# Kernel optimization log

Measured on AMD Instinct MI355X. Metric: run time of the kernel, lower is better.

Reference implementation:

```python
import jax, jax.numpy as jnp
import numpy as np

T = 5          # temporal_window_size
B = 512        # batch (graphs per timestep)
NA = 16        # num_agents (nodes per graph)
S = 64         # num_belief_states
A = 16         # action_dim
HID = 64       # hidden_dim per head
H = 4          # num_attn_heads
FD = HID * H   # 256, feature_dim
LAT = 128      # latent_dim
N = B * NA     # total nodes per timestep
FIN = S + A    # node feature dim
NEG_SLOPE = 0.2


def _edge_index():
    i, j = np.meshgrid(np.arange(NA), np.arange(NA), indexing='ij')
    m = i != j
    src_l, dst_l = i[m], j[m]                      # 240 intra-clique edges
    off = (np.arange(B) * NA)[:, None]
    src = (src_l[None] + off).ravel()
    dst = (dst_l[None] + off).ravel()
    loops = np.arange(N)                           # PyG GATConv add_self_loops=True
    src = np.concatenate([src, loops])
    dst = np.concatenate([dst, loops])
    return jnp.asarray(np.stack([src, dst]), dtype=jnp.int64)


def setup_inputs() -> dict:
    key = jax.random.key(0)
    ks = jax.random.split(key, 24)
    xav = lambda k, shp: jax.random.normal(k, shp, jnp.float32) * np.float32(np.sqrt(2.0 / (shp[0] + shp[-1])))
    return {
        'signals': jax.random.normal(ks[0], (T, B, S), jnp.float32),
        'neighbor_actions': jax.random.normal(ks[1], (T, B, NA * A), jnp.float32),
        'lin_w0': xav(ks[2], (FD, FIN)),
        'att_src0': xav(ks[3], (H, HID)),
        'att_dst0': xav(ks[4], (H, HID)),
        'bias0': jnp.zeros((FD,), jnp.float32),
        'lin_w1': xav(ks[5], (FD, FD)),
        'att_src1': xav(ks[6], (H, HID)),
        'att_dst1': xav(ks[7], (H, HID)),
        'bias1': jnp.zeros((FD,), jnp.float32),
        'in_proj_w': xav(ks[8], (3 * FD, FD)),
        'in_proj_b': jnp.zeros((3 * FD,), jnp.float32),
        'out_proj_w': xav(ks[9], (FD, FD)),
        'out_proj_b': jnp.zeros((FD,), jnp.float32),
        'w_mean': xav(ks[10], (LAT, FD)),
        'b_mean': jnp.zeros((LAT,), jnp.float32),
        'w_logvar': xav(ks[11], (LAT, FD)),
        'b_logvar': jnp.zeros((LAT,), jnp.float32),
        'w_belief': xav(ks[12], (S, FD)),
        'b_belief': jnp.zeros((S,), jnp.float32),
        'edge_index': _edge_index(),
    }


def _segment_softmax(e, seg, num_segments):
    # e: [E, T, H]; softmax over edges sharing the same target node.
    m = jax.ops.segment_max(e, seg, num_segments=num_segments)
    e = jnp.exp(e - m[seg])
    s = jax.ops.segment_sum(e, seg, num_segments=num_segments)
    return e / s[seg]


def _gat(x, src, dst, w, a_src, a_dst, b):
    # x: [N, T, Fin] -> [N, T, H*HID]   (PyG GATConv, concat heads)
    xl = jnp.einsum('ntf,of->nto', x, w).reshape(N, T, H, HID)
    e_src = jnp.einsum('nthc,hc->nth', xl, a_src)[src]   # [E, T, H]
    e_dst = jnp.einsum('nthc,hc->nth', xl, a_dst)[dst]
    e = jax.nn.leaky_relu(e_src + e_dst, NEG_SLOPE)
    alpha = _segment_softmax(e, dst, N)                  # per-target softmax
    out = jax.ops.segment_sum(alpha[..., None] * xl[src], dst, num_segments=N)
    return out.reshape(N, T, FD) + b


def reference(signals, neighbor_actions, lin_w0, att_src0, att_dst0, bias0,
              lin_w1, att_src1, att_dst1, bias1, in_proj_w, in_proj_b,
              out_proj_w, out_proj_b, w_mean, b_mean, w_logvar, b_logvar,
              w_belief, b_belief, edge_index):
    # --- _construct_graph (vectorized over time window + batch) ---
    acts = neighbor_actions.reshape(T, B, NA, A)
    beliefs = jnp.zeros((T, B, NA, S), signals.dtype).at[:, :, 0, :].set(signals)
    nodes = jnp.concatenate([beliefs, acts], -1).reshape(T, N, FIN)
    nodes = jnp.transpose(nodes, (1, 0, 2))              # [N, T, FIN]
    src, dst = edge_index[0], edge_index[1]
    x = jax.nn.relu(_gat(nodes, src, dst, lin_w0, att_src0, att_dst0, bias0))
    x = jax.nn.relu(_gat(x, src, dst, lin_w1, att_src1, att_dst1, bias1))
    # --- ego-node sequence: nodes 0, NA, 2*NA, ... ---
    seq = x[::NA]                                        # [B, T, FD]
    # --- temporal MultiheadAttention (batch_first, eval) ---
    qkv = seq @ in_proj_w.T + in_proj_b
    q, k, v = jnp.split(qkv, 3, axis=-1)
    dh = FD // H
    q = q.reshape(B, T, H, dh); k = k.reshape(B, T, H, dh); v = v.reshape(B, T, H, dh)
    scores = jnp.einsum('bqhd,bkhd->bhqk', q, k) / jnp.sqrt(jnp.asarray(dh, seq.dtype))
    # torch float attn_mask is ADDITIVE: mask[i,j]=1 if j<=i else 0
    mask = (jnp.arange(T)[:, None] >= jnp.arange(T)[None, :]).astype(seq.dtype)
    attn = jax.nn.softmax(scores + mask[None, None], axis=-1)
    ctx = jnp.einsum('bhqk,bkhd->bqhd', attn, v).reshape(B, T, FD)
    ctx = ctx @ out_proj_w.T + out_proj_b
    feat = ctx[:, -1]                                    # [B, FD]
    # --- heads ---
    mean = feat @ w_mean.T + b_mean
    logvar = feat @ w_logvar.T + b_logvar
    belief = jax.nn.softmax(feat @ w_belief.T + b_belief, axis=-1)
    return (mean, logvar, belief)
```

## Files before the change

kernel.cpp:

```cpp
#include <hip/hip_runtime.h>
#include <hip/hip_bf16.h>


__device__ __forceinline__ float wave_sum64(float v) {
    #pragma unroll
    for (int off = 32; off > 0; off >>= 1) v += __shfl_xor(v, off, 64);
    return v;
}
__device__ __forceinline__ float wave_max64(float v) {
    #pragma unroll
    for (int off = 32; off > 0; off >>= 1) v = fmaxf(v, __shfl_xor(v, off, 64));
    return v;
}

#define FMA4(acc, wv, zv) \
    acc = fmaf((wv).x, (zv).x, acc); acc = fmaf((wv).y, (zv).y, acc); \
    acc = fmaf((wv).z, (zv).z, acc); acc = fmaf((wv).w, (zv).w, acc);

__global__ __launch_bounds__(256) void k_pre(
    const float* __restrict__ w0, const float* __restrict__ w1,
    const float* __restrict__ wip, const float* __restrict__ wop,
    const float* __restrict__ wm, const float* __restrict__ wlv,
    const float* __restrict__ wb,
    const float* __restrict__ as0, const float* __restrict__ ad0,
    const float* __restrict__ as1, const float* __restrict__ ad1,
    float* __restrict__ tws,
    float* __restrict__ u1, float* __restrict__ ud1,
    float* __restrict__ pa0, float* __restrict__ pd0)
{
    const int tid = threadIdx.x;
    if (blockIdx.x < 1680) {
        int i = blockIdx.x * 256 + tid;
        float v; int d;
        if (i < 16384) {
            int k = i & 63, nn = i >> 6;
            v = w0[nn * 80 + k];
            d = (k >> 2) * 1024 + nn * 4 + (k & 3);
        } else if (i < 20480) {
            int j = i - 16384; int k = j & 15, nn = j >> 4;
            v = w0[nn * 80 + 64 + k];
            d = 16384 + (k >> 2) * 1024 + nn * 4 + (k & 3);
        } else if (i < 86016) {
            int j = i - 20480; int k = j & 255, nn = j >> 8;
            v = w1[nn * 256 + k];
            d = 20480 + (k >> 2) * 1024 + nn * 4 + (k & 3);
        } else if (i < 282624) {
            int j = i - 86016; int k = j & 255, nn = j >> 8;
            v = wip[nn * 256 + k];
            d = 86016 + (k >> 2) * 3072 + nn * 4 + (k & 3);
        } else if (i < 348160) {
            int j = i - 282624; int k = j & 255, nn = j >> 8;
            v = wop[nn * 256 + k];
            d = 282624 + (k >> 2) * 1024 + nn * 4 + (k & 3);
        } else {
            int j = i - 348160; int k = j & 255, o = j >> 8;
            if (o < 128)      v = wm[o * 256 + k];
            else if (o < 256) v = wlv[(o - 128) * 256 + k];
            else              v = wb[(o - 256) * 256 + k];
            d = 348160 + (k >> 2) * 1280 + o * 4 + (k & 3);
        }
        tws[d] = v;
        return;
    }
    if (blockIdx.x < 1684) {
        const int h = blockIdx.x - 1680;
        const int k = tid;
        float su = 0.f, sd = 0.f;
        #pragma unroll
        for (int c = 0; c < 64; c++) {
            float wv = w1[(h * 64 + c) * 256 + k];
            su = fmaf(as1[h * 64 + c], wv, su);
            sd = fmaf(ad1[h * 64 + c], wv, sd);
        }
        u1[h * 256 + k] = su;
        ud1[h * 256 + k] = sd;
        return;
    }
    if (tid < 64) {
        int h = tid >> 4, k = tid & 15;
        float su = 0.f, sd = 0.f;
        #pragma unroll
        for (int c = 0; c < 64; c++) {
            float wv = w0[(h * 64 + c) * 80 + 64 + k];
            su = fmaf(as0[h * 64 + c], wv, su);
            sd = fmaf(ad0[h * 64 + c], wv, sd);
        }
        pa0[tid] = su; pd0[tid] = sd;
    }
}

__global__ __launch_bounds__(256, 5) void k_gat(
    const float* __restrict__ sig,
    const float* __restrict__ nact,
    const float* __restrict__ W0sPK,
    const float* __restrict__ W0aPK,
    const float* __restrict__ W1PK,
    const float* __restrict__ u1g, const float* __restrict__ ud1g,
    const float* __restrict__ pa0g, const float* __restrict__ pd0g,
    const float* __restrict__ as0, const float* __restrict__ ad0,
    const float* __restrict__ b0, const float* __restrict__ b1,
    float* __restrict__ seqf)
{
    __shared__ __align__(16) char smem[28288];
    float* actL    = (float*)(smem + 0);
    float* sigL    = (float*)(smem + 1024);
    float* es0w    = (float*)(smem + 1280);
    float* ed0w    = (float*)(smem + 1536);
    float* espL    = (float*)(smem + 1792);
    float* es1L    = (float*)(smem + 2816);
    float* edpL    = (float*)(smem + 3072);
    float* alpha1L = (float*)(smem + 3136);
    float* a0L     = (float*)(smem + 3392);
    float* zL      = (float*)(smem + 7488);
    float* x1L     = (float*)(smem + 11648);

    const int tid = threadIdx.x;
    const int bg = blockIdx.x;
    const int b = bg / 5, g = bg - b * 5;
    const int n = tid, w = tid >> 6, lane = tid & 63;

    const float4* W0sPK4 = (const float4*)W0sPK;

    float4 wv0[8];
    #pragma unroll
    for (int j = 0; j < 8; j++) wv0[j] = W0sPK4[j * 256 + n];
    float4 wa[4];
    {
        const float4* W0aPK4 = (const float4*)W0aPK;
        #pragma unroll
        for (int q = 0; q < 4; q++) wa[q] = W0aPK4[q * 256 + n];
    }
    const float as0n = as0[n];
    const float ad0n = ad0[n];

    if (tid < 16)
        ((float4*)sigL)[tid] = ((const float4*)(sig + (g * 512 + b) * 64))[tid];
    if (tid < 64)
        ((float4*)actL)[tid] = ((const float4*)(nact + (g * 512 + b) * 256))[tid];
    __syncthreads();

    float S = 0.f;
    {
        const float4* sig4 = (const float4*)sigL;
        #pragma unroll
        for (int j = 0; j < 8; j++) {
            float4 sv = sig4[j];
            S = fmaf(wv0[j].x, sv.x, S);
            S = fmaf(wv0[j].y, sv.y, S);
            S = fmaf(wv0[j].z, sv.z, S);
            S = fmaf(wv0[j].w, sv.w, S);
        }
        float4 wv1[8];
        #pragma unroll
        for (int j = 0; j < 8; j++) wv1[j] = W0sPK4[(8 + j) * 256 + n];
        #pragma unroll
        for (int j = 0; j < 8; j++) {
            float4 sv = sig4[8 + j];
            S = fmaf(wv1[j].x, sv.x, S);
            S = fmaf(wv1[j].y, sv.y, S);
            S = fmaf(wv1[j].z, sv.z, S);
            S = fmaf(wv1[j].w, sv.w, S);
        }
    }
    const int m3 = lane >> 2, q3 = lane & 3;
    const float4 pv = ((const float4*)(pa0g + w * 16))[q3];
    const float4 dv = ((const float4*)(pd0g + w * 16))[q3];

    const float sS = wave_sum64(S * as0n);
    const float dS = wave_sum64(S * ad0n);

    {
        const float4 av = ((const float4*)(actL + m3 * 16))[q3];
        float su = av.x * pv.x;
        su = fmaf(av.y, pv.y, su); su = fmaf(av.z, pv.z, su); su = fmaf(av.w, pv.w, su);
        float sd = av.x * dv.x;
        sd = fmaf(av.y, dv.y, sd); sd = fmaf(av.z, dv.z, sd); sd = fmaf(av.w, dv.w, sd);
        su += __shfl_xor(su, 1, 64); su += __shfl_xor(su, 2, 64);
        sd += __shfl_xor(sd, 1, 64); sd += __shfl_xor(sd, 2, 64);
        if (q3 == 0) {
            es0w[w * 16 + m3] = su + ((m3 == 0) ? sS : 0.f);
            ed0w[w * 16 + m3] = sd + ((m3 == 0) ? dS : 0.f);
        }
    }
    {
        const int j = lane >> 2, q = lane & 3;
        const float ej = ed0w[w * 16 + j];
        const float4 ev = ((const float4*)(es0w + w * 16))[q];
        float e0 = ev.x + ej; e0 = (e0 >= 0.f) ? e0 : 0.2f * e0;
        float e1 = ev.y + ej; e1 = (e1 >= 0.f) ? e1 : 0.2f * e1;
        float e2 = ev.z + ej; e2 = (e2 >= 0.f) ? e2 : 0.2f * e2;
        float e3 = ev.w + ej; e3 = (e3 >= 0.f) ? e3 : 0.2f * e3;
        float mx = fmaxf(fmaxf(e0, e1), fmaxf(e2, e3));
        mx = fmaxf(mx, __shfl_xor(mx, 1, 64));
        mx = fmaxf(mx, __shfl_xor(mx, 2, 64));
        e0 = __expf(e0 - mx); e1 = __expf(e1 - mx);
        e2 = __expf(e2 - mx); e3 = __expf(e3 - mx);
        float s = e0 + e1 + e2 + e3;
        s += __shfl_xor(s, 1, 64); s += __shfl_xor(s, 2, 64);
        float inv = 1.f / s;
        ((float4*)(a0L + (w << 8) + j * 16))[q] =
            make_float4(e0 * inv, e1 * inv, e2 * inv, e3 * inv);
    }

    float x1r[16];
    {
        const float4* act4 = (const float4*)actL;
        float xl0r[16];
        #pragma unroll
        for (int s = 0; s < 16; s++) {
            float a = 0.f;
            #pragma unroll
            for (int q = 0; q < 4; q++) {
                float4 av = act4[s * 4 + q];
                FMA4(a, av, wa[q]);
            }
            xl0r[s] = a;
        }
        xl0r[0] += S;
        const float b0v = b0[n];
        const float4* a04 = (const float4*)(a0L + (w << 8));
        #pragma unroll
        for (int j = 0; j < 16; j++) {
            float acc = b0v;
            #pragma unroll
            for (int s4 = 0; s4 < 4; s4++) {
                float4 a4 = a04[j * 4 + s4];
                acc = fmaf(a4.x, xl0r[s4 * 4 + 0], acc);
                acc = fmaf(a4.y, xl0r[s4 * 4 + 1], acc);
                acc = fmaf(a4.z, xl0r[s4 * 4 + 2], acc);
                acc = fmaf(a4.w, xl0r[s4 * 4 + 3], acc);
            }
            x1r[j] = fmaxf(acc, 0.f);
            x1L[j * 260 + n] = x1r[j];
        }
    }
    __syncthreads();

    {
        const int m = tid & 15, h = (tid >> 4) & 3, p = tid >> 6;
        const float4* x4p = (const float4*)(x1L + m * 260 + p * 64);
        const float4* u4p = ((const float4*)u1g) + h * 64 + p * 16;
        float a = 0.f;
        #pragma unroll
        for (int i = 0; i < 16; i++) {
            float4 xv = x4p[i], uv = u4p[i];
            FMA4(a, xv, uv);
        }
        espL[m * 16 + h * 4 + p] = a;
        if (m == 0) {
            const float4* ud4p = ((const float4*)ud1g) + h * 64 + p * 16;
            float ad = 0.f;
            #pragma unroll
            for (int i = 0; i < 16; i++) {
                float4 xv = x4p[i], uv = ud4p[i];
                FMA4(ad, xv, uv);
            }
            edpL[h * 4 + p] = ad;
        }
    }
    __syncthreads();

    if (w == 0) {
        {
            const int m2 = lane >> 2, h = lane & 3;
            const float* e = espL + m2 * 16 + h * 4;
            es1L[m2 * 4 + h] = e[0] + e[1] + e[2] + e[3];
        }
        if (lane < 16) {
            const int h = lane >> 2, q = lane & 3;
            float ej = edpL[h * 4] + edpL[h * 4 + 1] + edpL[h * 4 + 2] + edpL[h * 4 + 3];
            float e[4]; float mx = -1e30f;
            #pragma unroll
            for (int r = 0; r < 4; r++) {
                float x = es1L[(q * 4 + r) * 4 + h] + ej;
                x = (x >= 0.f) ? x : 0.2f * x;
                e[r] = x; mx = fmaxf(mx, x);
            }
            mx = fmaxf(mx, __shfl_xor(mx, 1, 64));
            mx = fmaxf(mx, __shfl_xor(mx, 2, 64));
            float s = 0.f;
            #pragma unroll
            for (int r = 0; r < 4; r++) { e[r] = __expf(e[r] - mx); s += e[r]; }
            s += __shfl_xor(s, 1, 64);
            s += __shfl_xor(s, 2, 64);
            float inv = 1.f / s;
            ((float4*)(alpha1L + h * 16 + q * 4))[0] =
                make_float4(e[0] * inv, e[1] * inv, e[2] * inv, e[3] * inv);
        }
    }
    __syncthreads();

    const float4* W1PK4 = (const float4*)W1PK;
    float4 w1pf[8];
    #pragma unroll
    for (int j = 0; j < 8; j++) w1pf[j] = W1PK4[j * 256 + n];
    const float b1v = b1[n];
    {
        const float4* a14 = (const float4*)alpha1L;
        #pragma unroll
        for (int hh = 0; hh < 4; hh++) {
            float zv = 0.f;
            #pragma unroll
            for (int s4 = 0; s4 < 4; s4++) {
                float4 a4 = a14[hh * 4 + s4];
                zv = fmaf(a4.x, x1r[s4 * 4 + 0], zv);
                zv = fmaf(a4.y, x1r[s4 * 4 + 1], zv);
                zv = fmaf(a4.z, x1r[s4 * 4 + 2], zv);
                zv = fmaf(a4.w, x1r[s4 * 4 + 3], zv);
            }
            zL[hh * 260 + n] = zv;
        }
    }
    __syncthreads();

    {
        const float4* zh = (const float4*)(zL + w * 260);
        float acc = b1v;
        #pragma unroll
        for (int j = 0; j < 8; j++) {
            float4 z4 = zh[j];
            FMA4(acc, w1pf[j], z4);
        }
        #pragma unroll
        for (int io = 1; io < 8; io++) {
            float4 wv[8];
            #pragma unroll
            for (int j = 0; j < 8; j++) wv[j] = W1PK4[(io * 8 + j) * 256 + n];
            #pragma unroll
            for (int j = 0; j < 8; j++) {
                float4 z4 = zh[io * 8 + j];
                FMA4(acc, wv[j], z4);
            }
        }
        seqf[bg * 256 + n] = fmaxf(acc, 0.f);
    }
}

__global__ __launch_bounds__(768) void k_stage2(
    const float* __restrict__ seqf,
    const float* __restrict__ wipPK,
    const float* __restrict__ bip,
    const float* __restrict__ wopPK,
    const float* __restrict__ bop,
    const float* __restrict__ whPK,
    const float* __restrict__ bm, const float* __restrict__ blv,
    const float* __restrict__ bb,
    float* __restrict__ out)
{
    __shared__ float sseq[2][5][256];
    __shared__ float kL[2][5][256], vL[2][5][256], qL[2][256];
    __shared__ float ctxL[2][256], featL[2][256];
    __shared__ float beliefL[2][64];
    const int tid = threadIdx.x;
    const int b0 = blockIdx.x * 2;

    {
        float4* sflat = (float4*)&sseq[0][0][0];
        const float4* src = (const float4*)(seqf + b0 * 1280);
        if (tid < 640) sflat[tid] = src[tid];
    }
    __syncthreads();

    {
        const int kind = tid >> 8, n = tid & 255;
        const float4* wPK = (const float4*)wipPK + tid;
        if (kind == 0) {
            const float4* s0 = (const float4*)&sseq[0][4][0];
            const float4* s1 = (const float4*)&sseq[1][4][0];
            float a0 = 0.f, a1 = 0.f;
            #pragma unroll 8
            for (int k4 = 0; k4 < 64; k4++) {
                float4 wv = wPK[k4 * 768];
                float4 x0 = s0[k4], x1 = s1[k4];
                a0 = fmaf(x0.x, wv.x, a0); a0 = fmaf(x0.y, wv.y, a0);
                a0 = fmaf(x0.z, wv.z, a0); a0 = fmaf(x0.w, wv.w, a0);
                a1 = fmaf(x1.x, wv.x, a1); a1 = fmaf(x1.y, wv.y, a1);
                a1 = fmaf(x1.z, wv.z, a1); a1 = fmaf(x1.w, wv.w, a1);
            }
            float bv = bip[n];
            qL[0][n] = a0 + bv; qL[1][n] = a1 + bv;
        } else {
            float acc[2][5] = {{0.f,0.f,0.f,0.f,0.f},{0.f,0.f,0.f,0.f,0.f}};
            #pragma unroll 4
            for (int k4 = 0; k4 < 64; k4++) {
                float4 wv = wPK[k4 * 768];
                #pragma unroll
                for (int gb = 0; gb < 2; gb++) {
                    #pragma unroll
                    for (int t = 0; t < 5; t++) {
                        float4 sv = ((const float4*)&sseq[gb][t][0])[k4];
                        float a = acc[gb][t];
                        a = fmaf(sv.x, wv.x, a); a = fmaf(sv.y, wv.y, a);
                        a = fmaf(sv.z, wv.z, a); a = fmaf(sv.w, wv.w, a);
                        acc[gb][t] = a;
                    }
                }
            }
            float bv = bip[kind * 256 + n];
            float* dst = (kind == 1) ? &kL[0][0][0] : &vL[0][0][0];
            #pragma unroll
            for (int gb = 0; gb < 2; gb++)
                #pragma unroll
                for (int t = 0; t < 5; t++)
                    dst[gb * 1280 + t * 256 + n] = acc[gb][t] + bv;
        }
    }
    __syncthreads();

    if (tid < 512) {
        const int gb = tid >> 8, col = tid & 255;
        float q4 = qL[gb][col];
        float sc[5];
        #pragma unroll
        for (int t = 0; t < 5; t++)
            sc[t] = wave_sum64(q4 * kL[gb][t][col]) * 0.125f;
        float m = sc[0];
        #pragma unroll
        for (int t = 1; t < 5; t++) m = fmaxf(m, sc[t]);
        float p[5], sum = 0.f;
        #pragma unroll
        for (int t = 0; t < 5; t++) { p[t] = __expf(sc[t] - m); sum += p[t]; }
        float inv = 1.f / sum, cv = 0.f;
        #pragma unroll
        for (int t = 0; t < 5; t++) cv = fmaf(p[t], vL[gb][t][col], cv);
        ctxL[gb][col] = cv * inv;
    }
    __syncthreads();

    if (tid < 512) {
        const int gb = tid >> 8, n = tid & 255;
        const float4* wPK = (const float4*)wopPK + n;
        const float4* c4 = (const float4*)&ctxL[gb][0];
        float acc = 0.f;
        #pragma unroll 8
        for (int k4 = 0; k4 < 64; k4++) {
            float4 wv = wPK[k4 * 256], cv = c4[k4];
            FMA4(acc, wv, cv);
        }
        featL[gb][n] = acc + bop[n];
    }
    __syncthreads();

    if (tid < 640) {
        const int gb = tid / 320, j = tid - gb * 320;
        const float4* wPK = (const float4*)whPK + j;
        const float4* f4 = (const float4*)&featL[gb][0];
        float acc = 0.f;
        #pragma unroll 8
        for (int k4 = 0; k4 < 64; k4++) {
            float4 wv = wPK[k4 * 320], fv = f4[k4];
            FMA4(acc, wv, fv);
        }
        if (j < 128) {
            out[(b0 + gb) * 128 + j] = acc + bm[j];
        } else if (j < 256) {
            out[65536 + (b0 + gb) * 128 + (j - 128)] = acc + blv[j - 128];
        } else {
            beliefL[gb][j - 256] = acc + bb[j - 256];
        }
    }
    __syncthreads();

    if (tid < 128) {
        int gb = tid >> 6, lane = tid & 63;
        float lg = beliefL[gb][lane];
        float m = wave_max64(lg);
        float e = __expf(lg - m);
        float s = wave_sum64(e);
        out[131072 + (b0 + gb) * 64 + lane] = e / s;
    }
}

extern "C" void kernel_launch(void* const* d_in, const int* in_sizes, int n_in,
                              void* d_out, int out_size, void* d_ws, size_t ws_size,
                              hipStream_t stream) {
    const float* sig  = (const float*)d_in[0];
    const float* nact = (const float*)d_in[1];
    const float* w0   = (const float*)d_in[2];
    const float* as0  = (const float*)d_in[3];
    const float* ad0  = (const float*)d_in[4];
    const float* b0   = (const float*)d_in[5];
    const float* w1   = (const float*)d_in[6];
    const float* as1  = (const float*)d_in[7];
    const float* ad1  = (const float*)d_in[8];
    const float* b1   = (const float*)d_in[9];
    const float* wip  = (const float*)d_in[10];
    const float* bip  = (const float*)d_in[11];
    const float* wop  = (const float*)d_in[12];
    const float* bop  = (const float*)d_in[13];
    const float* wm   = (const float*)d_in[14];
    const float* bm   = (const float*)d_in[15];
    const float* wlv  = (const float*)d_in[16];
    const float* blv  = (const float*)d_in[17];
    const float* wb   = (const float*)d_in[18];
    const float* bb   = (const float*)d_in[19];

    float* ws    = (float*)d_ws;
    float* seqf  = ws;
    float* tws   = ws + 655360;
    float* W0sPK = tws;
    float* W0aPK = tws + 16384;
    float* W1PK  = tws + 20480;
    float* wipPK = tws + 86016;
    float* wopPK = tws + 282624;
    float* whPK  = tws + 348160;
    float* u1    = ws + 1085440;
    float* ud1   = ws + 1086464;
    float* pa0   = ws + 1087488;
    float* pd0   = ws + 1087552;

    k_pre   <<<1685, 256, 0, stream>>>(w0, w1, wip, wop, wm, wlv, wb,
                                       as0, ad0, as1, ad1,
                                       tws, u1, ud1, pa0, pd0);
    k_gat   <<<2560, 256, 0, stream>>>(sig, nact, W0sPK, W0aPK, W1PK,
                                       u1, ud1, pa0, pd0, as0, ad0, b0, b1, seqf);
    k_stage2<<<256, 768, 0, stream>>>(seqf, wipPK, bip, wopPK, bop, whPK,
                                      bm, blv, bb, (float*)d_out);
}
```

Measured before the change: 182.4 us.

## Restructure stage2 to 256 threads computing Q/K/V in registers per column

The temporal-attention kernel now runs 256 threads per block instead of 768, and each thread computes the Q, K and V projections for its column in registers. The attention scores are then reduced across waves directly from those registers, so the K/V/Q shared-memory staging and one barrier go away. In exchange each thread does three times the projection work, holds more registers, and the block has less parallelism to hide weight-load latency. The belief head is handled by the first 64 threads in a separate loop.

```diff
diff --git a/kernel.cpp b/kernel.cpp
--- a/kernel.cpp
+++ b/kernel.cpp
@@ -336,7 +336,7 @@
     }
 }
 
-__global__ __launch_bounds__(768) void k_stage2(
+__global__ __launch_bounds__(256) void k_stage2(
     const float* __restrict__ seqf,
     const float* __restrict__ wipPK,
     const float* __restrict__ bip,
@@ -348,115 +348,116 @@
     float* __restrict__ out)
 {
     __shared__ float sseq[2][5][256];
-    __shared__ float kL[2][5][256], vL[2][5][256], qL[2][256];
-    __shared__ float ctxL[2][256], featL[2][256];
+    __shared__ float ctxL[2][256];
+    __shared__ float featL[2][256];
     __shared__ float beliefL[2][64];
     const int tid = threadIdx.x;
     const int b0 = blockIdx.x * 2;
 
     {
-        float4* sflat = (float4*)&sseq[0][0][0];
+        float4* sf = (float4*)&sseq[0][0][0];
         const float4* src = (const float4*)(seqf + b0 * 1280);
-        if (tid < 640) sflat[tid] = src[tid];
-    }
-    __syncthreads();
-
-    {
-        const int kind = tid >> 8, n = tid & 255;
-        const float4* wPK = (const float4*)wipPK + tid;
-        if (kind == 0) {
-            const float4* s0 = (const float4*)&sseq[0][4][0];
-            const float4* s1 = (const float4*)&sseq[1][4][0];
-            float a0 = 0.f, a1 = 0.f;
+        #pragma unroll
+        for (int r = 0; r < 2; r++) sf[r * 256 + tid] = src[r * 256 + tid];
+        if (tid < 128) sf[512 + tid] = src[512 + tid];
+    }
+    __syncthreads();
+
+    float qa[2] = {0.f, 0.f};
+    float ka[2][5] = {{0,0,0,0,0},{0,0,0,0,0}};
+    float va[2][5] = {{0,0,0,0,0},{0,0,0,0,0}};
+    {
+        const float4* x4 = (const float4*)&sseq[0][0][0];
+        const float4* wqp = (const float4*)wipPK + tid;
+        const float4* wkp = wqp + 256;
+        const float4* wvp = wqp + 512;
+        #pragma unroll 2
+        for (int k4 = 0; k4 < 64; k4++) {
+            float4 wqv = wqp[k4 * 768];
+            float4 wkv = wkp[k4 * 768];
+            float4 wvv = wvp[k4 * 768];
+            #pragma unroll
+            for (int gb = 0; gb < 2; gb++) {
+                #pragma unroll
+                for (int t = 0; t < 5; t++) {
+                    float4 xv = x4[gb * 320 + t * 64 + k4];
+                    FMA4(ka[gb][t], wkv, xv);
+                    FMA4(va[gb][t], wvv, xv);
+                    if (t == 4) FMA4(qa[gb], wqv, xv);
+                }
+            }
+        }
+        const float bq = bip[tid], bk = bip[256 + tid], bv = bip[512 + tid];
+        #pragma unroll
+        for (int gb = 0; gb < 2; gb++) {
+            qa[gb] += bq;
+            #pragma unroll
+            for (int t = 0; t < 5; t++) { ka[gb][t] += bk; va[gb][t] += bv; }
+        }
+    }
+
+    #pragma unroll
+    for (int gb = 0; gb < 2; gb++) {
+        float sc[5];
+        #pragma unroll
+        for (int t = 0; t < 5; t++)
+            sc[t] = wave_sum64(qa[gb] * ka[gb][t]) * 0.125f;
+        float m = sc[0];
+        #pragma unroll
+        for (int t = 1; t < 5; t++) m = fmaxf(m, sc[t]);
+        float p[5], sum = 0.f;
+        #pragma unroll
+        for (int t = 0; t < 5; t++) { p[t] = __expf(sc[t] - m); sum += p[t]; }
+        float inv = 1.f / sum, cv = 0.f;
+        #pragma unroll
+        for (int t = 0; t < 5; t++) cv = fmaf(p[t], va[gb][t], cv);
+        ctxL[gb][tid] = cv * inv;
+    }
+    __syncthreads();
+
+    {
+        const float4* wPK = (const float4*)wopPK + tid;
+        #pragma unroll
+        for (int gb = 0; gb < 2; gb++) {
+            const float4* c4 = (const float4*)&ctxL[gb][0];
+            float acc = 0.f;
             #pragma unroll 8
             for (int k4 = 0; k4 < 64; k4++) {
-                float4 wv = wPK[k4 * 768];
-                float4 x0 = s0[k4], x1 = s1[k4];
-                a0 = fmaf(x0.x, wv.x, a0); a0 = fmaf(x0.y, wv.y, a0);
-                a0 = fmaf(x0.z, wv.z, a0); a0 = fmaf(x0.w, wv.w, a0);
-                a1 = fmaf(x1.x, wv.x, a1); a1 = fmaf(x1.y, wv.y, a1);
-                a1 = fmaf(x1.z, wv.z, a1); a1 = fmaf(x1.w, wv.w, a1);
-            }
-            float bv = bip[n];
-            qL[0][n] = a0 + bv; qL[1][n] = a1 + bv;
-        } else {
-            float acc[2][5] = {{0.f,0.f,0.f,0.f,0.f},{0.f,0.f,0.f,0.f,0.f}};
-            #pragma unroll 4
+                float4 wv = wPK[k4 * 256], cv = c4[k4];
+                FMA4(acc, wv, cv);
+            }
+            featL[gb][tid] = acc + bop[tid];
+        }
+    }
+    __syncthreads();
+
+    {
+        const float4* wPK = (const float4*)whPK + tid;
+        #pragma unroll
+        for (int gb = 0; gb < 2; gb++) {
+            const float4* f4 = (const float4*)&featL[gb][0];
+            float acc = 0.f;
+            #pragma unroll 8
             for (int k4 = 0; k4 < 64; k4++) {
-                float4 wv = wPK[k4 * 768];
-                #pragma unroll
-                for (int gb = 0; gb < 2; gb++) {
-                    #pragma unroll
-                    for (int t = 0; t < 5; t++) {
-                        float4 sv = ((const float4*)&sseq[gb][t][0])[k4];
-                        float a = acc[gb][t];
-                        a = fmaf(sv.x, wv.x, a); a = fmaf(sv.y, wv.y, a);
-                        a = fmaf(sv.z, wv.z, a); a = fmaf(sv.w, wv.w, a);
-                        acc[gb][t] = a;
-                    }
+                float4 wv = wPK[k4 * 320], fv = f4[k4];
+                FMA4(acc, wv, fv);
+            }
+            if (tid < 128) out[(b0 + gb) * 128 + tid] = acc + bm[tid];
+            else out[65536 + (b0 + gb) * 128 + (tid - 128)] = acc + blv[tid - 128];
+        }
+        if (tid < 64) {
+            const float4* w2 = (const float4*)whPK + 256 + tid;
+            #pragma unroll
+            for (int gb = 0; gb < 2; gb++) {
+                const float4* f4 = (const float4*)&featL[gb][0];
+                float acc2 = 0.f;
+                #pragma unroll 8
+                for (int k4 = 0; k4 < 64; k4++) {
+                    float4 wv = w2[k4 * 320], fv = f4[k4];
+                    FMA4(acc2, wv, fv);
                 }
-            }
-            float bv = bip[kind * 256 + n];
-            float* dst = (kind == 1) ? &kL[0][0][0] : &vL[0][0][0];
-            #pragma unroll
-            for (int gb = 0; gb < 2; gb++)
-                #pragma unroll
-                for (int t = 0; t < 5; t++)
-                    dst[gb * 1280 + t * 256 + n] = acc[gb][t] + bv;
-        }
-    }
-    __syncthreads();
-
-    if (tid < 512) {
-        const int gb = tid >> 8, col = tid & 255;
-        float q4 = qL[gb][col];
-        float sc[5];
-        #pragma unroll
-        for (int t = 0; t < 5; t++)
-            sc[t] = wave_sum64(q4 * kL[gb][t][col]) * 0.125f;
-        float m = sc[0];
-        #pragma unroll
-        for (int t = 1; t < 5; t++) m = fmaxf(m, sc[t]);
-        float p[5], sum = 0.f;
-        #pragma unroll
-        for (int t = 0; t < 5; t++) { p[t] = __expf(sc[t] - m); sum += p[t]; }
-        float inv = 1.f / sum, cv = 0.f;
-        #pragma unroll
-        for (int t = 0; t < 5; t++) cv = fmaf(p[t], vL[gb][t][col], cv);
-        ctxL[gb][col] = cv * inv;
-    }
-    __syncthreads();
-
-    if (tid < 512) {
-        const int gb = tid >> 8, n = tid & 255;
-        const float4* wPK = (const float4*)wopPK + n;
-        const float4* c4 = (const float4*)&ctxL[gb][0];
-        float acc = 0.f;
-        #pragma unroll 8
-        for (int k4 = 0; k4 < 64; k4++) {
-            float4 wv = wPK[k4 * 256], cv = c4[k4];
-            FMA4(acc, wv, cv);
-        }
-        featL[gb][n] = acc + bop[n];
-    }
-    __syncthreads();
-
-    if (tid < 640) {
-        const int gb = tid / 320, j = tid - gb * 320;
-        const float4* wPK = (const float4*)whPK + j;
-        const float4* f4 = (const float4*)&featL[gb][0];
-        float acc = 0.f;
-        #pragma unroll 8
-        for (int k4 = 0; k4 < 64; k4++) {
-            float4 wv = wPK[k4 * 320], fv = f4[k4];
-            FMA4(acc, wv, fv);
-        }
-        if (j < 128) {
-            out[(b0 + gb) * 128 + j] = acc + bm[j];
-        } else if (j < 256) {
-            out[65536 + (b0 + gb) * 128 + (j - 128)] = acc + blv[j - 128];
-        } else {
-            beliefL[gb][j - 256] = acc + bb[j - 256];
+                beliefL[gb][tid] = acc2 + bb[tid];
+            }
         }
     }
     __syncthreads();
@@ -514,6 +515,6 @@
                                        tws, u1, ud1, pa0, pd0);
     k_gat   <<<2560, 256, 0, stream>>>(sig, nact, W0sPK, W0aPK, W1PK,
                                        u1, ud1, pa0, pd0, as0, ad0, b0, b1, seqf);
-    k_stage2<<<256, 768, 0, stream>>>(seqf, wipPK, bip, wopPK, bop, whPK,
+    k_stage2<<<256, 256, 0, stream>>>(seqf, wipPK, bip, wopPK, bop, whPK,
                                       bm, blv, bb, (float*)d_out);
 }
```

New measurement: 204.2 us. 11.9% more time.

## Process two batch graphs per GAT block to reuse loaded weights

Applied to the files above, without the earlier changes.

Each k_gat block now handles two graphs (two batch indices at the same timestep) instead of one, and the grid is halved. The per-thread weight registers for W0 and the streamed W1 rows are shared across both graphs, so each weight is fetched once and used twice. The final W1 projection accumulates both graphs in one pass. The cost is more shared memory, more registers (launch bounds drop from 5 to 4 blocks per CU), fewer blocks, and a serial loop over the two graphs for the attention stages.

```diff
diff --git a/kernel.cpp b/kernel.cpp
--- a/kernel.cpp
+++ b/kernel.cpp
@@ -89,7 +89,7 @@
     }
 }
 
-__global__ __launch_bounds__(256, 5) void k_gat(
+__global__ __launch_bounds__(256, 4) void k_gat(
     const float* __restrict__ sig,
     const float* __restrict__ nact,
     const float* __restrict__ W0sPK,
@@ -101,25 +101,26 @@
     const float* __restrict__ b0, const float* __restrict__ b1,
     float* __restrict__ seqf)
 {
-    __shared__ __align__(16) char smem[28288];
-    float* actL    = (float*)(smem + 0);
-    float* sigL    = (float*)(smem + 1024);
-    float* es0w    = (float*)(smem + 1280);
-    float* ed0w    = (float*)(smem + 1536);
-    float* espL    = (float*)(smem + 1792);
-    float* es1L    = (float*)(smem + 2816);
-    float* edpL    = (float*)(smem + 3072);
-    float* alpha1L = (float*)(smem + 3136);
-    float* a0L     = (float*)(smem + 3392);
-    float* zL      = (float*)(smem + 7488);
-    float* x1L     = (float*)(smem + 11648);
+    __shared__ __align__(16) char smem[35136];
+    float* actL  = (float*)(smem + 0);
+    float* sigL  = (float*)(smem + 2048);
+    float* es0w  = (float*)(smem + 2560);
+    float* ed0w  = (float*)(smem + 2816);
+    float* espL  = (float*)(smem + 3072);
+    float* edpL  = (float*)(smem + 4096);
+    float* es1w  = (float*)(smem + 4160);
+    float* alphw = (float*)(smem + 5184);
+    float* a0L   = (float*)(smem + 6208);
+    float* x1L   = (float*)(smem + 10304);
+    float* zL    = (float*)(smem + 26944);
 
     const int tid = threadIdx.x;
-    const int bg = blockIdx.x;
-    const int b = bg / 5, g = bg - b * 5;
+    const int blk = blockIdx.x;
+    const int p = blk / 5, g = blk - p * 5;
     const int n = tid, w = tid >> 6, lane = tid & 63;
 
     const float4* W0sPK4 = (const float4*)W0sPK;
+    const float4* W1PK4  = (const float4*)W1PK;
 
     float4 wv0[8];
     #pragma unroll
@@ -133,206 +134,215 @@
     const float as0n = as0[n];
     const float ad0n = ad0[n];
 
-    if (tid < 16)
-        ((float4*)sigL)[tid] = ((const float4*)(sig + (g * 512 + b) * 64))[tid];
-    if (tid < 64)
-        ((float4*)actL)[tid] = ((const float4*)(nact + (g * 512 + b) * 256))[tid];
+    if (tid < 32) {
+        int pr = tid >> 4, q = tid & 15;
+        ((float4*)sigL)[tid] =
+            ((const float4*)sig)[(g * 512 + 2 * p + pr) * 16 + q];
+    }
+    if (tid < 128) {
+        int pr = tid >> 6, q = tid & 63;
+        ((float4*)actL)[tid] =
+            ((const float4*)nact)[(g * 512 + 2 * p + pr) * 64 + q];
+    }
     __syncthreads();
 
-    float S = 0.f;
+    float SA = 0.f, SB = 0.f;
     {
         const float4* sig4 = (const float4*)sigL;
         #pragma unroll
         for (int j = 0; j < 8; j++) {
-            float4 sv = sig4[j];
-            S = fmaf(wv0[j].x, sv.x, S);
-            S = fmaf(wv0[j].y, sv.y, S);
-            S = fmaf(wv0[j].z, sv.z, S);
-            S = fmaf(wv0[j].w, sv.w, S);
+            float4 wv = wv0[j];
+            float4 va = sig4[j], vb = sig4[16 + j];
+            FMA4(SA, wv, va); FMA4(SB, wv, vb);
         }
         float4 wv1[8];
         #pragma unroll
         for (int j = 0; j < 8; j++) wv1[j] = W0sPK4[(8 + j) * 256 + n];
         #pragma unroll
         for (int j = 0; j < 8; j++) {
-            float4 sv = sig4[8 + j];
-            S = fmaf(wv1[j].x, sv.x, S);
-            S = fmaf(wv1[j].y, sv.y, S);
-            S = fmaf(wv1[j].z, sv.z, S);
-            S = fmaf(wv1[j].w, sv.w, S);
+            float4 wv = wv1[j];
+            float4 va = sig4[8 + j], vb = sig4[24 + j];
+            FMA4(SA, wv, va); FMA4(SB, wv, vb);
         }
     }
     const int m3 = lane >> 2, q3 = lane & 3;
     const float4 pv = ((const float4*)(pa0g + w * 16))[q3];
     const float4 dv = ((const float4*)(pd0g + w * 16))[q3];
-
-    const float sS = wave_sum64(S * as0n);
-    const float dS = wave_sum64(S * ad0n);
-
-    {
-        const float4 av = ((const float4*)(actL + m3 * 16))[q3];
-        float su = av.x * pv.x;
-        su = fmaf(av.y, pv.y, su); su = fmaf(av.z, pv.z, su); su = fmaf(av.w, pv.w, su);
-        float sd = av.x * dv.x;
-        sd = fmaf(av.y, dv.y, sd); sd = fmaf(av.z, dv.z, sd); sd = fmaf(av.w, dv.w, sd);
-        su += __shfl_xor(su, 1, 64); su += __shfl_xor(su, 2, 64);
-        sd += __shfl_xor(sd, 1, 64); sd += __shfl_xor(sd, 2, 64);
-        if (q3 == 0) {
-            es0w[w * 16 + m3] = su + ((m3 == 0) ? sS : 0.f);
-            ed0w[w * 16 + m3] = sd + ((m3 == 0) ? dS : 0.f);
-        }
-    }
-    {
-        const int j = lane >> 2, q = lane & 3;
-        const float ej = ed0w[w * 16 + j];
-        const float4 ev = ((const float4*)(es0w + w * 16))[q];
-        float e0 = ev.x + ej; e0 = (e0 >= 0.f) ? e0 : 0.2f * e0;
-        float e1 = ev.y + ej; e1 = (e1 >= 0.f) ? e1 : 0.2f * e1;
-        float e2 = ev.z + ej; e2 = (e2 >= 0.f) ? e2 : 0.2f * e2;
-        float e3 = ev.w + ej; e3 = (e3 >= 0.f) ? e3 : 0.2f * e3;
-        float mx = fmaxf(fmaxf(e0, e1), fmaxf(e2, e3));
-        mx = fmaxf(mx, __shfl_xor(mx, 1, 64));
-        mx = fmaxf(mx, __shfl_xor(mx, 2, 64));
-        e0 = __expf(e0 - mx); e1 = __expf(e1 - mx);
-        e2 = __expf(e2 - mx); e3 = __expf(e3 - mx);
-        float s = e0 + e1 + e2 + e3;
-        s += __shfl_xor(s, 1, 64); s += __shfl_xor(s, 2, 64);
-        float inv = 1.f / s;
-        ((float4*)(a0L + (w << 8) + j * 16))[q] =
-            make_float4(e0 * inv, e1 * inv, e2 * inv, e3 * inv);
-    }
-
-    float x1r[16];
-    {
-        const float4* act4 = (const float4*)actL;
-        float xl0r[16];
-        #pragma unroll
-        for (int s = 0; s < 16; s++) {
-            float a = 0.f;
-            #pragma unroll
-            for (int q = 0; q < 4; q++) {
-                float4 av = act4[s * 4 + q];
-                FMA4(a, av, wa[q]);
-            }
-            xl0r[s] = a;
-        }
-        xl0r[0] += S;
-        const float b0v = b0[n];
-        const float4* a04 = (const float4*)(a0L + (w << 8));
-        #pragma unroll
-        for (int j = 0; j < 16; j++) {
-            float acc = b0v;
-            #pragma unroll
-            for (int s4 = 0; s4 < 4; s4++) {
-                float4 a4 = a04[j * 4 + s4];
-                acc = fmaf(a4.x, xl0r[s4 * 4 + 0], acc);
-                acc = fmaf(a4.y, xl0r[s4 * 4 + 1], acc);
-                acc = fmaf(a4.z, xl0r[s4 * 4 + 2], acc);
-                acc = fmaf(a4.w, xl0r[s4 * 4 + 3], acc);
-            }
-            x1r[j] = fmaxf(acc, 0.f);
-            x1L[j * 260 + n] = x1r[j];
-        }
-    }
-    __syncthreads();
-
-    {
-        const int m = tid & 15, h = (tid >> 4) & 3, p = tid >> 6;
-        const float4* x4p = (const float4*)(x1L + m * 260 + p * 64);
-        const float4* u4p = ((const float4*)u1g) + h * 64 + p * 16;
-        float a = 0.f;
-        #pragma unroll
-        for (int i = 0; i < 16; i++) {
-            float4 xv = x4p[i], uv = u4p[i];
-            FMA4(a, xv, uv);
-        }
-        espL[m * 16 + h * 4 + p] = a;
-        if (m == 0) {
-            const float4* ud4p = ((const float4*)ud1g) + h * 64 + p * 16;
-            float ad = 0.f;
-            #pragma unroll
-            for (int i = 0; i < 16; i++) {
-                float4 xv = x4p[i], uv = ud4p[i];
-                FMA4(ad, xv, uv);
-            }
-            edpL[h * 4 + p] = ad;
-        }
-    }
-    __syncthreads();
-
-    if (w == 0) {
-        {
-            const int m2 = lane >> 2, h = lane & 3;
-            const float* e = espL + m2 * 16 + h * 4;
-            es1L[m2 * 4 + h] = e[0] + e[1] + e[2] + e[3];
-        }
-        if (lane < 16) {
-            const int h = lane >> 2, q = lane & 3;
-            float ej = edpL[h * 4] + edpL[h * 4 + 1] + edpL[h * 4 + 2] + edpL[h * 4 + 3];
-            float e[4]; float mx = -1e30f;
-            #pragma unroll
-            for (int r = 0; r < 4; r++) {
-                float x = es1L[(q * 4 + r) * 4 + h] + ej;
-                x = (x >= 0.f) ? x : 0.2f * x;
-                e[r] = x; mx = fmaxf(mx, x);
-            }
-            mx = fmaxf(mx, __shfl_xor(mx, 1, 64));
-            mx = fmaxf(mx, __shfl_xor(mx, 2, 64));
-            float s = 0.f;
-            #pragma unroll
-            for (int r = 0; r < 4; r++) { e[r] = __expf(e[r] - mx); s += e[r]; }
-            s += __shfl_xor(s, 1, 64);
-            s += __shfl_xor(s, 2, 64);
-            float inv = 1.f / s;
-            ((float4*)(alpha1L + h * 16 + q * 4))[0] =
-                make_float4(e[0] * inv, e[1] * inv, e[2] * inv, e[3] * inv);
-        }
-    }
-    __syncthreads();
-
-    const float4* W1PK4 = (const float4*)W1PK;
+    const float b0v = b0[n];
+    const float b1v = b1[n];
     float4 w1pf[8];
     #pragma unroll
     for (int j = 0; j < 8; j++) w1pf[j] = W1PK4[j * 256 + n];
-    const float b1v = b1[n];
+
+    float Scur = SA;
+    #pragma unroll 1
+    for (int pr = 0; pr < 2; pr++) {
+        const float sS = wave_sum64(Scur * as0n);
+        const float dS = wave_sum64(Scur * ad0n);
+
+        {
+            const float4 av =
+                ((const float4*)(actL + (pr << 8) + m3 * 16))[q3];
+            float su = av.x * pv.x;
+            su = fmaf(av.y, pv.y, su); su = fmaf(av.z, pv.z, su); su = fmaf(av.w, pv.w, su);
+            float sd = av.x * dv.x;
+            sd = fmaf(av.y, dv.y, sd); sd = fmaf(av.z, dv.z, sd); sd = fmaf(av.w, dv.w, sd);
+            su += __shfl_xor(su, 1, 64); su += __shfl_xor(su, 2, 64);
+            sd += __shfl_xor(sd, 1, 64); sd += __shfl_xor(sd, 2, 64);
+            if (q3 == 0) {
+                es0w[w * 16 + m3] = su + ((m3 == 0) ? sS : 0.f);
+                ed0w[w * 16 + m3] = sd + ((m3 == 0) ? dS : 0.f);
+            }
+        }
+        {
+            const int j = lane >> 2, q = lane & 3;
+            const float ej = ed0w[w * 16 + j];
+            const float4 ev = ((const float4*)(es0w + w * 16))[q];
+            float e0 = ev.x + ej; e0 = (e0 >= 0.f) ? e0 : 0.2f * e0;
+            float e1 = ev.y + ej; e1 = (e1 >= 0.f) ? e1 : 0.2f * e1;
+            float e2 = ev.z + ej; e2 = (e2 >= 0.f) ? e2 : 0.2f * e2;
+            float e3 = ev.w + ej; e3 = (e3 >= 0.f) ? e3 : 0.2f * e3;
+            float mx = fmaxf(fmaxf(e0, e1), fmaxf(e2, e3));
+            mx = fmaxf(mx, __shfl_xor(mx, 1, 64));
+            mx = fmaxf(mx, __shfl_xor(mx, 2, 64));
+            e0 = __expf(e0 - mx); e1 = __expf(e1 - mx);
+            e2 = __expf(e2 - mx); e3 = __expf(e3 - mx);
+            float s = e0 + e1 + e2 + e3;
+            s += __shfl_xor(s, 1, 64); s += __shfl_xor(s, 2, 64);
+            float inv = 1.f / s;
+            ((float4*)(a0L + (w << 8) + j * 16))[q] =
+                make_float4(e0 * inv, e1 * inv, e2 * inv, e3 * inv);
+        }
+
+        float x1r[16];
+        {
+            const float4* act4 = (const float4*)(actL + (pr << 8));
+            float xl0r[16];
+            #pragma unroll
+            for (int s = 0; s < 16; s++) {
+                float a = 0.f;
+                #pragma unroll
+                for (int q = 0; q < 4; q++) {
+                    float4 av = act4[s * 4 + q];
+                    FMA4(a, av, wa[q]);
+                }
+                xl0r[s] = a;
+            }
+            xl0r[0] += Scur;
+            const float4* a04 = (const float4*)(a0L + (w << 8));
+            #pragma unroll
+            for (int j = 0; j < 16; j++) {
+                float acc = b0v;
+                #pragma unroll
+                for (int s4 = 0; s4 < 4; s4++) {
+                    float4 a4 = a04[j * 4 + s4];
+                    acc = fmaf(a4.x, xl0r[s4 * 4 + 0], acc);
+                    acc = fmaf(a4.y, xl0r[s4 * 4 + 1], acc);
+                    acc = fmaf(a4.z, xl0r[s4 * 4 + 2], acc);
+                    acc = fmaf(a4.w, xl0r[s4 * 4 + 3], acc);
+                }
+                x1r[j] = fmaxf(acc, 0.f);
+                x1L[j * 260 + n] = x1r[j];
+            }
+        }
+        __syncthreads();
+
+        {
+            const int m = tid & 15, h = (tid >> 4) & 3, pch = tid >> 6;
+            const float4* x4p = (const float4*)(x1L + m * 260 + pch * 64);
+            const float4* u4p = ((const float4*)u1g) + h * 64 + pch * 16;
+            float a = 0.f;
+            #pragma unroll
+            for (int i = 0; i < 16; i++) {
+                float4 xv = x4p[i], uv = u4p[i];
+                FMA4(a, xv, uv);
+            }
+            espL[m * 16 + h * 4 + pch] = a;
+            if (m == 0) {
+                const float4* ud4p = ((const float4*)ud1g) + h * 64 + pch * 16;
+                float ad = 0.f;
+                #pragma unroll
+                for (int i = 0; i < 16; i++) {
+                    float4 xv = x4p[i], uv = ud4p[i];
+                    FMA4(ad, xv, uv);
+                }
+                edpL[h * 4 + pch] = ad;
+            }
+        }
+        __syncthreads();
+
+        {
+            const int m2 = lane >> 2, h2 = lane & 3;
+            const float* e = espL + m2 * 16 + h2 * 4;
+            es1w[(w << 6) + lane] = e[0] + e[1] + e[2] + e[3];
+            if (lane < 16) {
+                const int h = lane >> 2, q = lane & 3;
+                float ej = edpL[h * 4] + edpL[h * 4 + 1]
+                         + edpL[h * 4 + 2] + edpL[h * 4 + 3];
+                float ev[4]; float mx = -1e30f;
+                #pragma unroll
+                for (int r = 0; r < 4; r++) {
+                    float x = es1w[(w << 6) + (q * 4 + r) * 4 + h] + ej;
+                    x = (x >= 0.f) ? x : 0.2f * x;
+                    ev[r] = x; mx = fmaxf(mx, x);
+                }
+                mx = fmaxf(mx, __shfl_xor(mx, 1, 64));
+                mx = fmaxf(mx, __shfl_xor(mx, 2, 64));
+                float s = 0.f;
+                #pragma unroll
+                for (int r = 0; r < 4; r++) { ev[r] = __expf(ev[r] - mx); s += ev[r]; }
+                s += __shfl_xor(s, 1, 64);
+                s += __shfl_xor(s, 2, 64);
+                float inv = 1.f / s;
+                ((float4*)(alphw + (w << 6) + h * 16 + q * 4))[0] =
+                    make_float4(ev[0] * inv, ev[1] * inv, ev[2] * inv, ev[3] * inv);
+            }
+        }
+        {
+            const float4* a14 = (const float4*)(alphw + (w << 6));
+            float* zg = zL + (pr << 10);
+            #pragma unroll
+            for (int hh = 0; hh < 4; hh++) {
+                float zv = 0.f;
+                #pragma unroll
+                for (int s4 = 0; s4 < 4; s4++) {
+                    float4 a4 = a14[hh * 4 + s4];
+                    zv = fmaf(a4.x, x1r[s4 * 4 + 0], zv);
+                    zv = fmaf(a4.y, x1r[s4 * 4 + 1], zv);
+                    zv = fmaf(a4.z, x1r[s4 * 4 + 2], zv);
+                    zv = fmaf(a4.w, x1r[s4 * 4 + 3], zv);
+                }
+                zg[hh * 256 + n] = zv;
+            }
+        }
+        __syncthreads();
+        Scur = SB;
+    }
+
     {
-        const float4* a14 = (const float4*)alpha1L;
-        #pragma unroll
-        for (int hh = 0; hh < 4; hh++) {
-            float zv = 0.f;
-            #pragma unroll
-            for (int s4 = 0; s4 < 4; s4++) {
-                float4 a4 = a14[hh * 4 + s4];
-                zv = fmaf(a4.x, x1r[s4 * 4 + 0], zv);
-                zv = fmaf(a4.y, x1r[s4 * 4 + 1], zv);
-                zv = fmaf(a4.z, x1r[s4 * 4 + 2], zv);
-                zv = fmaf(a4.w, x1r[s4 * 4 + 3], zv);
-            }
-            zL[hh * 260 + n] = zv;
-        }
-    }
-    __syncthreads();
-
-    {
-        const float4* zh = (const float4*)(zL + w * 260);
-        float acc = b1v;
+        const float4* zL4 = (const float4*)zL;
+        const int zb = w << 6;
+        float aA = b1v, aB = b1v;
         #pragma unroll
         for (int j = 0; j < 8; j++) {
-            float4 z4 = zh[j];
-            FMA4(acc, w1pf[j], z4);
-        }
-        #pragma unroll
+            float4 wv = w1pf[j];
+            float4 zA = zL4[zb + j], zB = zL4[256 + zb + j];
+            FMA4(aA, wv, zA); FMA4(aB, wv, zB);
+        }
+        #pragma unroll 1
         for (int io = 1; io < 8; io++) {
-            float4 wv[8];
-            #pragma unroll
-            for (int j = 0; j < 8; j++) wv[j] = W1PK4[(io * 8 + j) * 256 + n];
+            float4 wv2[8];
+            #pragma unroll
+            for (int j = 0; j < 8; j++) wv2[j] = W1PK4[((io * 8 + j) << 8) + n];
             #pragma unroll
             for (int j = 0; j < 8; j++) {
-                float4 z4 = zh[io * 8 + j];
-                FMA4(acc, wv[j], z4);
-            }
-        }
-        seqf[bg * 256 + n] = fmaxf(acc, 0.f);
+                const int k4 = io * 8 + j;
+                float4 zA = zL4[zb + k4], zB = zL4[256 + zb + k4];
+                FMA4(aA, wv2[j], zA); FMA4(aB, wv2[j], zB);
+            }
+        }
+        seqf[(p * 10 + g) * 256 + n]     = fmaxf(aA, 0.f);
+        seqf[(p * 10 + 5 + g) * 256 + n] = fmaxf(aB, 0.f);
     }
 }
 
@@ -512,7 +522,7 @@
     k_pre   <<<1685, 256, 0, stream>>>(w0, w1, wip, wop, wm, wlv, wb,
                                        as0, ad0, as1, ad1,
                                        tws, u1, ud1, pa0, pd0);
-    k_gat   <<<2560, 256, 0, stream>>>(sig, nact, W0sPK, W0aPK, W1PK,
+    k_gat   <<<1280, 256, 0, stream>>>(sig, nact, W0sPK, W0aPK, W1PK,
                                        u1, ud1, pa0, pd0, as0, ad0, b0, b1, seqf);
     k_stage2<<<256, 768, 0, stream>>>(seqf, wipPK, bip, wopPK, bop, whPK,
                                       bm, blv, bb, (float*)d_out);
```

New measurement: 226.5 us. 1.24x slower.
